# Kernel optimization log

Hardware: AMD Instinct MI355X
Metric: run time of the kernel (lower is better)

Reference implementation:

```python
import jax, jax.numpy as jnp
import numpy as np

W_BIT = 4
OUT_F = 11008
IN_F = 4096
K = 16


def unpack_sign(q_bytes):
    """q_bytes: [n_bytes] int32 holding uint8 values. Little-endian bit order.
    Returns float32 signs in {-1, +1} of shape [OUT_F, IN_F]."""
    bits = (q_bytes[:, None] >> jnp.arange(8, dtype=q_bytes.dtype)) & 1  # [n_bytes, 8]
    signs = (2 * bits - 1).astype(jnp.float32)
    return signs.reshape(OUT_F, IN_F)


def setup_inputs() -> dict:
    key = jax.random.key(0)
    k0, k1, k2, k3 = jax.random.split(key, 4)
    x = jax.random.normal(k0, (4, 2048, IN_F), dtype=jnp.float32)
    # packed sign bits: one byte stores 8 signs; OUT_F*IN_F//8 bytes per bit-plane
    qweight = jax.random.randint(k1, (W_BIT, OUT_F * IN_F // 8), 0, 256, dtype=jnp.int32)
    u = jax.random.normal(k2, (W_BIT, OUT_F, K), dtype=jnp.float32) * 0.05
    vt = jax.random.normal(k3, (W_BIT, K, IN_F), dtype=jnp.float32) * 0.05
    return {"x": x, "qweight": qweight, "u": u, "vt": vt}


def reference(x, qweight, u, vt):
    # Reconstruct full weight: w = sum_i sign_i * (u_i @ vt_i), then GEMM x @ w.T.
    # Loop over the small fixed w_bit count to avoid holding all [OUT,IN] bit-planes at once.
    w = jnp.zeros((OUT_F, IN_F), dtype=x.dtype)
    for i in range(W_BIT):
        signs = unpack_sign(qweight[i])            # [OUT_F, IN_F]
        w = w + signs * (u[i] @ vt[i])             # rank-K reconstruction masked by signs
    return x @ w.T                                  # [B, S, OUT_F]
```

## Files before the change

### kernel.cpp

```cpp
#include <hip/hip_runtime.h>
#include <hip/hip_bf16.h>

#define W_BIT 4
#define OUT_F 11008
#define IN_F 4096
#define KRANK 16
#define M_DIM 8192
#define QW_PLANE (OUT_F * IN_F / 8)

#define N_DIM OUT_F
#define K_DIM 4096
#define NT 64
#define NBN 43
#define RW_BLOCKS 5504
#define CV_BLOCKS 1024

typedef __attribute__((ext_vector_type(8))) short short8;
typedef __attribute__((ext_vector_type(4))) float f32x4;

__device__ __forceinline__ short f2bf(float f) {
    union { float f; unsigned u; } v;
    v.f = f;
    unsigned r = v.u + 0x7fffu + ((v.u >> 16) & 1u);
    return (short)(r >> 16);
}

__device__ __forceinline__ void async16(void* lds_p, const void* g) {
    __builtin_amdgcn_global_load_lds(
        (const __attribute__((address_space(1))) unsigned int*)g,
        (__attribute__((address_space(3))) unsigned int*)lds_p,
        16, 0, 0);
}

#define BAR() __builtin_amdgcn_s_barrier()
#define LGKM(n) do { asm volatile("s_waitcnt lgkmcnt(" #n ")" ::: "memory"); \
                     __builtin_amdgcn_sched_barrier(0); } while (0)
#define VMC(n) do { asm volatile("s_waitcnt vmcnt(" #n ")" ::: "memory"); \
                    __builtin_amdgcn_sched_barrier(0); } while (0)
#define PRIO1() __builtin_amdgcn_s_setprio(1)
#define PRIO0() __builtin_amdgcn_s_setprio(0)

#define DSR(DST, AV, IMM) \
    asm volatile("ds_read_b128 %0, %1 offset:%2" : "=v"(DST) : "v"(AV), "n"(IMM))

__global__ __launch_bounds__(256) void prep_kernel(
    const float* __restrict__ x, const int* __restrict__ qw,
    const float* __restrict__ u, const float* __restrict__ vt,
    short* __restrict__ xb, short* __restrict__ wb) {
    const int b = blockIdx.x;
    const int t = threadIdx.x;

    if (b >= RW_BLOCKS) {
        const int n8 = (M_DIM * IN_F) / 8;
        int tid = (b - RW_BLOCKS) * 256 + t;
        for (int i = tid; i < n8; i += CV_BLOCKS * 256) {
            f32x4 a = ((const f32x4*)x)[2 * i];
            f32x4 c = ((const f32x4*)x)[2 * i + 1];
            short8 o;
            o[0] = f2bf(a[0]); o[1] = f2bf(a[1]); o[2] = f2bf(a[2]); o[3] = f2bf(a[3]);
            o[4] = f2bf(c[0]); o[5] = f2bf(c[1]); o[6] = f2bf(c[2]); o[7] = f2bf(c[3]);
            ((short8*)xb)[i] = o;
        }
        return;
    }

    __shared__ float vts[64][128];
    __shared__ float us[64][64];

    const int c0 = (b & 31) * 128;
    const int o0 = (b >> 5) * 64;

    {
        const f32x4* vt4 = (const f32x4*)vt;
        const int l32 = t & 31;
        const int r0w = t >> 5;
#pragma unroll
        for (int j = 0; j < 8; ++j) {
            int row = r0w + j * 8;
            ((f32x4*)&vts[row][0])[l32] = vt4[(size_t)row * 1024 + (c0 >> 2) + l32];
        }
    }
    {
        const int o = t & 63, q = t >> 6;
#pragma unroll
        for (int i = 0; i < 4; ++i) {
            f32x4 v = ((const f32x4*)u)[((size_t)i * OUT_F + o0 + o) * 4 + q];
            us[i * 16 + q * 4 + 0][o] = v[0];
            us[i * 16 + q * 4 + 1][o] = v[1];
            us[i * 16 + q * 4 + 2][o] = v[2];
            us[i * 16 + q * 4 + 3][o] = v[3];
        }
    }
    __syncthreads();

    const int to = (t >> 4) * 4;
    const int tc = (t & 15) * 8;

    float wacc[4][8];
#pragma unroll
    for (int r = 0; r < 4; ++r)
#pragma unroll
        for (int c = 0; c < 8; ++c) wacc[r][c] = 0.f;

#pragma unroll
    for (int i = 0; i < W_BIT; ++i) {
        float dot[4][8];
#pragma unroll
        for (int r = 0; r < 4; ++r)
#pragma unroll
            for (int c = 0; c < 8; ++c) dot[r][c] = 0.f;
#pragma unroll
        for (int k = 0; k < KRANK; ++k) {
            f32x4 uv = *(const f32x4*)&us[i * 16 + k][to];
            f32x4 v0 = *(const f32x4*)&vts[i * 16 + k][tc];
            f32x4 v1 = *(const f32x4*)&vts[i * 16 + k][tc + 4];
#pragma unroll
            for (int r = 0; r < 4; ++r) {
#pragma unroll
                for (int c = 0; c < 4; ++c) {
                    dot[r][c]     += uv[r] * v0[c];
                    dot[r][c + 4] += uv[r] * v1[c];
                }
            }
        }
#pragma unroll
        for (int r = 0; r < 4; ++r) {
            unsigned byte = (unsigned)qw[i * QW_PLANE + (((o0 + to + r) * IN_F + c0 + tc) >> 3)];
#pragma unroll
            for (int c = 0; c < 8; ++c)
                wacc[r][c] += ((byte >> c) & 1u) ? dot[r][c] : -dot[r][c];
        }
    }
#pragma unroll
    for (int r = 0; r < 4; ++r) {
        short8 o8;
#pragma unroll
        for (int c = 0; c < 8; ++c) o8[c] = f2bf(wacc[r][c]);
        *(short8*)&wb[(size_t)(o0 + to + r) * IN_F + c0 + tc] = o8;
    }
}

__global__ __launch_bounds__(512, 2) void gemm256_kernel(
    const short* __restrict__ A, const short* __restrict__ B, float* __restrict__ C) {
    extern __shared__ short lds[];

    const int t = threadIdx.x;
    const int lane = t & 63, wid = t >> 6;
    const int wr = wid >> 2, wc = wid & 3;
    const int fr = lane & 15, fq = lane >> 4;

    const int bid = blockIdx.x;
    const int cpx = gridDim.x >> 3;
    const int swzb = (bid & 7) * cpx + (bid >> 3);
    const int bm = swzb / NBN, bn = swzb % NBN;
    const long row0 = (long)bm * 256, col0 = (long)bn * 256;

    const int colswz = (fq ^ ((fr >> 1) & 3)) * 8;
    const int aoff = (wr * 128 + fr) * 32 + colswz;
    const int boff = 32768 + (wc * 64 + fr) * 32 + colswz;

    const unsigned av = (unsigned)(size_t)((__attribute__((address_space(3))) short*)lds + aoff);
    const unsigned bv = (unsigned)(size_t)((__attribute__((address_space(3))) short*)lds + boff);

    const int srow = t >> 2;
    const int sswz = (((t & 3) ^ ((srow >> 1) & 3)) << 3);
    const short* pA0 = A + (row0 + srow) * (size_t)K_DIM + sswz;
    const short* pA1 = pA0 + (size_t)128 * K_DIM;
    const short* pB0 = B + (col0 + srow) * (size_t)K_DIM + sswz;
    const short* pB1 = pB0 + (size_t)128 * K_DIM;
    const int ldst0 = t * 8;

    f32x4 acc[8][4];
#pragma unroll
    for (int m = 0; m < 8; ++m)
#pragma unroll
        for (int n = 0; n < 4; ++n) acc[m][n] = (f32x4)0.f;

    short8 afA[4], afB[4], bf0[4], bf1[4];

#define STG(P0, P1, SLOT, OFFB) do {                                   \
    async16(&lds[(SLOT) + ldst0], (const char*)(P0) + (OFFB));         \
    async16(&lds[(SLOT) + 4096 + ldst0], (const char*)(P1) + (OFFB));  \
} while (0)

#define RDA(SET, KSLOT, MH) do {                                       \
    DSR(SET[0], av, ((KSLOT) + ((MH) * 4 + 0) * 512) * 2);             \
    DSR(SET[1], av, ((KSLOT) + ((MH) * 4 + 1) * 512) * 2);             \
    DSR(SET[2], av, ((KSLOT) + ((MH) * 4 + 2) * 512) * 2);             \
    DSR(SET[3], av, ((KSLOT) + ((MH) * 4 + 3) * 512) * 2);             \
} while (0)

#define RDB(DST, KSLOT) do {                                           \
    DSR(DST[0], bv, ((KSLOT) - 32768 + 0 * 512) * 2);                  \
    DSR(DST[1], bv, ((KSLOT) - 32768 + 1 * 512) * 2);                  \
    DSR(DST[2], bv, ((KSLOT) - 32768 + 2 * 512) * 2);                  \
    DSR(DST[3], bv, ((KSLOT) - 32768 + 3 * 512) * 2);                  \
} while (0)

#define MMA(AF, BF, MH) do { PRIO1();                                  \
    _Pragma("unroll") for (int m = 0; m < 4; ++m)                      \
        _Pragma("unroll") for (int n = 0; n < 4; ++n)                  \
            acc[(MH) * 4 + m][n] = __builtin_amdgcn_mfma_f32_16x16x32_bf16( \
                AF[m], BF[n], acc[(MH) * 4 + m][n], 0, 0, 0);          \
    PRIO0(); __builtin_amdgcn_sched_barrier(0); } while (0)

    STG(pA0, pA1, 0,     0);
    STG(pB0, pB1, 32768, 0);
    STG(pA0, pA1, 8192,  64);
    STG(pB0, pB1, 40960, 64);
    STG(pA0, pA1, 16384, 128);
    STG(pB0, pB1, 49152, 128);
    VMC(4);
    BAR();
    RDA(afA, 0, 0); RDB(bf0, 32768);

    for (int it = 0; it < 31; ++it) {
        RDA(afB, 0, 1);
        STG(pA0, pA1, 24576, 192);
        BAR(); LGKM(4); MMA(afA, bf0, 0);
        RDB(bf1, 40960); RDA(afA, 8192, 0);
        STG(pB0, pB1, 57344, 192);
        BAR(); LGKM(8); MMA(afB, bf0, 1);
        RDA(afB, 8192, 1);
        STG(pA0, pA1, 0, 256);
        BAR(); LGKM(4); MMA(afA, bf1, 0);
        STG(pB0, pB1, 32768, 256);
        VMC(4);
        RDB(bf0, 49152); RDA(afA, 16384, 0);
        BAR(); LGKM(8); MMA(afB, bf1, 1);

        RDA(afB, 16384, 1);
        STG(pA0, pA1, 8192, 320);
        BAR(); LGKM(4); MMA(afA, bf0, 0);
        RDB(bf1, 57344); RDA(afA, 24576, 0);
        STG(pB0, pB1, 40960, 320);
        BAR(); LGKM(8); MMA(afB, bf0, 1);
        RDA(afB, 24576, 1);
        STG(pA0, pA1, 16384, 384);
        BAR(); LGKM(4); MMA(afA, bf1, 0);
        STG(pB0, pB1, 49152, 384);
        VMC(4);
        RDB(bf0, 32768); RDA(afA, 0, 0);
        BAR(); LGKM(8); MMA(afB, bf1, 1);

        pA0 += 128; pA1 += 128; pB0 += 128; pB1 += 128;
    }

    RDA(afB, 0, 1);
    STG(pA0, pA1, 24576, 192);
    BAR(); LGKM(4); MMA(afA, bf0, 0);
    RDB(bf1, 40960); RDA(afA, 8192, 0);
    STG(pB0, pB1, 57344, 192);
    BAR(); LGKM(8); MMA(afB, bf0, 1);
    RDA(afB, 8192, 1);
    BAR(); LGKM(4); MMA(afA, bf1, 0);
    VMC(0);
    RDB(bf0, 49152); RDA(afA, 16384, 0);
    BAR(); LGKM(8); MMA(afB, bf1, 1);
    RDA(afB, 16384, 1);
    BAR(); LGKM(4); MMA(afA, bf0, 0);
    RDB(bf1, 57344); RDA(afA, 24576, 0);
    BAR(); LGKM(8); MMA(afB, bf0, 1);
    RDA(afB, 24576, 1);
    BAR(); LGKM(4); MMA(afA, bf1, 0);
    BAR(); LGKM(0); MMA(afB, bf1, 1);

#pragma unroll
    for (int m = 0; m < 8; ++m) {
#pragma unroll
        for (int n = 0; n < 4; ++n) {
            f32x4 v = acc[m][n];
            long r0 = row0 + wr * 128 + m * 16 + fq * 4;
            long cc = col0 + wc * 64 + n * 16 + fr;
#pragma unroll
            for (int jj = 0; jj < 4; ++jj)
                C[(size_t)(r0 + jj) * N_DIM + cc] = v[jj];
        }
    }
#undef STG
#undef RDA
#undef RDB
#undef MMA
}

extern "C" void kernel_launch(void* const* d_in, const int* in_sizes, int n_in,
                              void* d_out, int out_size, void* d_ws, size_t ws_size,
                              hipStream_t stream) {
    const float* x  = (const float*)d_in[0];
    const int*   qw = (const int*)d_in[1];
    const float* u  = (const float*)d_in[2];
    const float* vt = (const float*)d_in[3];
    float* out = (float*)d_out;

    const size_t wb_bytes = (size_t)OUT_F * IN_F * 2;
    short* wb = (short*)d_ws;
    short* xb = (short*)((char*)d_ws + wb_bytes);

    (void)hipFuncSetAttribute((const void*)gemm256_kernel,
                              hipFuncAttributeMaxDynamicSharedMemorySize, 131072);

    hipLaunchKernelGGL(prep_kernel, dim3(RW_BLOCKS + CV_BLOCKS), dim3(256), 0, stream,
                       x, qw, u, vt, xb, wb);
    hipLaunchKernelGGL(gemm256_kernel, dim3((M_DIM / 256) * (N_DIM / 256)), dim3(512), 131072,
                       stream, xb, wb, out);
}
```

Baseline: 855.9 us.

## Switch GEMM main loop to BK=64 double-buffered LDS tiles with 8-way swizzle

Reworks the bf16 GEMM mainloop from four 32-wide K slots to two 64-wide K stages (ping-pong), staging 64-column rows with an 8-group XOR swizzle and issuing two MFMAs per accumulator per quarter-tile. Intent is fewer barriers and prefetch phases per K step and larger loads per stage, cutting sync overhead. It adds more barriers per quadrant, waits for all LDS reads (lgkmcnt 0) before each MFMA block, and uses more fragment registers, which can reduce latency hiding.

```diff
diff --git a/kernel.cpp b/kernel.cpp
--- a/kernel.cpp
+++ b/kernel.cpp
@@ -10,7 +10,6 @@
 
 #define N_DIM OUT_F
 #define K_DIM 4096
-#define NT 64
 #define NBN 43
 #define RW_BLOCKS 5504
 #define CV_BLOCKS 1024
@@ -33,7 +32,7 @@
 }
 
 #define BAR() __builtin_amdgcn_s_barrier()
-#define LGKM(n) do { asm volatile("s_waitcnt lgkmcnt(" #n ")" ::: "memory"); \
+#define LGKM0() do { asm volatile("s_waitcnt lgkmcnt(0)" ::: "memory"); \
                      __builtin_amdgcn_sched_barrier(0); } while (0)
 #define VMC(n) do { asm volatile("s_waitcnt vmcnt(" #n ")" ::: "memory"); \
                     __builtin_amdgcn_sched_barrier(0); } while (0)
@@ -155,20 +154,19 @@
     const int bm = swzb / NBN, bn = swzb % NBN;
     const long row0 = (long)bm * 256, col0 = (long)bn * 256;
 
-    const int colswz = (fq ^ ((fr >> 1) & 3)) * 8;
-    const int aoff = (wr * 128 + fr) * 32 + colswz;
-    const int boff = 32768 + (wc * 64 + fr) * 32 + colswz;
-
-    const unsigned av = (unsigned)(size_t)((__attribute__((address_space(3))) short*)lds + aoff);
-    const unsigned bv = (unsigned)(size_t)((__attribute__((address_space(3))) short*)lds + boff);
-
-    const int srow = t >> 2;
-    const int sswz = (((t & 3) ^ ((srow >> 1) & 3)) << 3);
-    const short* pA0 = A + (row0 + srow) * (size_t)K_DIM + sswz;
-    const short* pA1 = pA0 + (size_t)128 * K_DIM;
-    const short* pB0 = B + (col0 + srow) * (size_t)K_DIM + sswz;
-    const short* pB1 = pB0 + (size_t)128 * K_DIM;
-    const int ldst0 = t * 8;
+    const int f7 = fr & 7;
+    const int g0 = fq ^ f7;
+    const int g1 = (4 + fq) ^ f7;
+    const int arow = (wr * 128 + fr) * 64;
+    const int brow = (wc * 64 + fr) * 64;
+    const unsigned av0 = (unsigned)(size_t)((__attribute__((address_space(3))) short*)lds + arow + g0 * 8);
+    const unsigned av1 = (unsigned)(size_t)((__attribute__((address_space(3))) short*)lds + arow + g1 * 8);
+    const unsigned bv0 = (unsigned)(size_t)((__attribute__((address_space(3))) short*)lds + 32768 + brow + g0 * 8);
+    const unsigned bv1 = (unsigned)(size_t)((__attribute__((address_space(3))) short*)lds + 32768 + brow + g1 * 8);
+
+    const int sswz = (((t & 7) ^ ((t >> 3) & 7)) << 3);
+    const short* pA = A + (row0 + (t >> 3)) * (size_t)K_DIM + sswz;
+    const short* pB = B + (col0 + (t >> 3)) * (size_t)K_DIM + sswz;
 
     f32x4 acc[8][4];
 #pragma unroll
@@ -176,94 +174,97 @@
 #pragma unroll
         for (int n = 0; n < 4; ++n) acc[m][n] = (f32x4)0.f;
 
-    short8 afA[4], afB[4], bf0[4], bf1[4];
-
-#define STG(P0, P1, SLOT, OFFB) do {                                   \
-    async16(&lds[(SLOT) + ldst0], (const char*)(P0) + (OFFB));         \
-    async16(&lds[(SLOT) + 4096 + ldst0], (const char*)(P1) + (OFFB));  \
-} while (0)
-
-#define RDA(SET, KSLOT, MH) do {                                       \
-    DSR(SET[0], av, ((KSLOT) + ((MH) * 4 + 0) * 512) * 2);             \
-    DSR(SET[1], av, ((KSLOT) + ((MH) * 4 + 1) * 512) * 2);             \
-    DSR(SET[2], av, ((KSLOT) + ((MH) * 4 + 2) * 512) * 2);             \
-    DSR(SET[3], av, ((KSLOT) + ((MH) * 4 + 3) * 512) * 2);             \
-} while (0)
-
-#define RDB(DST, KSLOT) do {                                           \
-    DSR(DST[0], bv, ((KSLOT) - 32768 + 0 * 512) * 2);                  \
-    DSR(DST[1], bv, ((KSLOT) - 32768 + 1 * 512) * 2);                  \
-    DSR(DST[2], bv, ((KSLOT) - 32768 + 2 * 512) * 2);                  \
-    DSR(DST[3], bv, ((KSLOT) - 32768 + 3 * 512) * 2);                  \
-} while (0)
-
-#define MMA(AF, BF, MH) do { PRIO1();                                  \
-    _Pragma("unroll") for (int m = 0; m < 4; ++m)                      \
-        _Pragma("unroll") for (int n = 0; n < 4; ++n)                  \
-            acc[(MH) * 4 + m][n] = __builtin_amdgcn_mfma_f32_16x16x32_bf16( \
-                AF[m], BF[n], acc[(MH) * 4 + m][n], 0, 0, 0);          \
+    short8 a0[8], a1[8], b0[4], b1[4];
+
+#define STGA(P, H, OFFB) do {                                               \
+    async16(&lds[(P) * 16384 + (2 * (H)) * 4096 + t * 8],                   \
+            (const char*)(pA + (size_t)(2 * (H)) * 64 * K_DIM) + (OFFB));   \
+    async16(&lds[(P) * 16384 + (2 * (H) + 1) * 4096 + t * 8],               \
+            (const char*)(pA + (size_t)(2 * (H) + 1) * 64 * K_DIM) + (OFFB)); \
+} while (0)
+#define STGB(P, H, OFFB) do {                                               \
+    async16(&lds[32768 + (P) * 16384 + (2 * (H)) * 4096 + t * 8],           \
+            (const char*)(pB + (size_t)(2 * (H)) * 64 * K_DIM) + (OFFB));   \
+    async16(&lds[32768 + (P) * 16384 + (2 * (H) + 1) * 4096 + t * 8],       \
+            (const char*)(pB + (size_t)(2 * (H) + 1) * 64 * K_DIM) + (OFFB)); \
+} while (0)
+
+#define RDA(SET, P, MH) do {                                                \
+    DSR(SET[0], av0, ((P) * 16384 + (MH) * 4096 + 0 * 1024) * 2);           \
+    DSR(SET[1], av0, ((P) * 16384 + (MH) * 4096 + 1 * 1024) * 2);           \
+    DSR(SET[2], av0, ((P) * 16384 + (MH) * 4096 + 2 * 1024) * 2);           \
+    DSR(SET[3], av0, ((P) * 16384 + (MH) * 4096 + 3 * 1024) * 2);           \
+    DSR(SET[4], av1, ((P) * 16384 + (MH) * 4096 + 0 * 1024) * 2);           \
+    DSR(SET[5], av1, ((P) * 16384 + (MH) * 4096 + 1 * 1024) * 2);           \
+    DSR(SET[6], av1, ((P) * 16384 + (MH) * 4096 + 2 * 1024) * 2);           \
+    DSR(SET[7], av1, ((P) * 16384 + (MH) * 4096 + 3 * 1024) * 2);           \
+} while (0)
+
+#define RDB(SET, P, NH) do {                                                \
+    DSR(SET[0], bv0, ((P) * 16384 + (NH) * 2048 + 0 * 1024) * 2);           \
+    DSR(SET[1], bv0, ((P) * 16384 + (NH) * 2048 + 1 * 1024) * 2);           \
+    DSR(SET[2], bv1, ((P) * 16384 + (NH) * 2048 + 0 * 1024) * 2);           \
+    DSR(SET[3], bv1, ((P) * 16384 + (NH) * 2048 + 1 * 1024) * 2);           \
+} while (0)
+
+#define MMAQ(ASET, BSET, MH, NH) do { PRIO1();                              \
+    _Pragma("unroll") for (int m = 0; m < 4; ++m)                           \
+        _Pragma("unroll") for (int n = 0; n < 2; ++n) {                     \
+            acc[(MH) * 4 + m][(NH) * 2 + n] =                               \
+                __builtin_amdgcn_mfma_f32_16x16x32_bf16(                    \
+                    ASET[m], BSET[n], acc[(MH) * 4 + m][(NH) * 2 + n], 0, 0, 0); \
+            acc[(MH) * 4 + m][(NH) * 2 + n] =                               \
+                __builtin_amdgcn_mfma_f32_16x16x32_bf16(                    \
+                    ASET[4 + m], BSET[2 + n], acc[(MH) * 4 + m][(NH) * 2 + n], 0, 0, 0); \
+        }                                                                   \
     PRIO0(); __builtin_amdgcn_sched_barrier(0); } while (0)
 
-    STG(pA0, pA1, 0,     0);
-    STG(pB0, pB1, 32768, 0);
-    STG(pA0, pA1, 8192,  64);
-    STG(pB0, pB1, 40960, 64);
-    STG(pA0, pA1, 16384, 128);
-    STG(pB0, pB1, 49152, 128);
+#define TILE(P, OFFB, OFFA) do {                                            \
+                                                          \
+    RDA(a0, P, 0); RDB(b0, P, 0);                                           \
+    STGB(1 - (P), 0, OFFB);                                                 \
+    BAR(); LGKM0(); MMAQ(a0, b0, 0, 0); BAR();                              \
+                                                          \
+    RDA(a1, P, 1);                                                          \
+    STGB(1 - (P), 1, OFFB);                                                 \
+    BAR(); LGKM0(); MMAQ(a1, b0, 1, 0); BAR();                              \
+                                                          \
+    RDB(b1, P, 1);                                                          \
+    STGA(P, 0, OFFA);                                                       \
+    BAR(); LGKM0(); MMAQ(a1, b1, 1, 1); BAR();                              \
+                             \
+    STGA(P, 1, OFFA);                                                       \
+    BAR(); MMAQ(a0, b1, 0, 1); VMC(4); BAR();                               \
+} while (0)
+
+    STGA(0, 0, 0); STGA(0, 1, 0);
+    STGB(0, 0, 0); STGB(0, 1, 0);
+    STGA(1, 0, 128); STGA(1, 1, 128);
     VMC(4);
     BAR();
-    RDA(afA, 0, 0); RDB(bf0, 32768);
 
     for (int it = 0; it < 31; ++it) {
-        RDA(afB, 0, 1);
-        STG(pA0, pA1, 24576, 192);
-        BAR(); LGKM(4); MMA(afA, bf0, 0);
-        RDB(bf1, 40960); RDA(afA, 8192, 0);
-        STG(pB0, pB1, 57344, 192);
-        BAR(); LGKM(8); MMA(afB, bf0, 1);
-        RDA(afB, 8192, 1);
-        STG(pA0, pA1, 0, 256);
-        BAR(); LGKM(4); MMA(afA, bf1, 0);
-        STG(pB0, pB1, 32768, 256);
-        VMC(4);
-        RDB(bf0, 49152); RDA(afA, 16384, 0);
-        BAR(); LGKM(8); MMA(afB, bf1, 1);
-
-        RDA(afB, 16384, 1);
-        STG(pA0, pA1, 8192, 320);
-        BAR(); LGKM(4); MMA(afA, bf0, 0);
-        RDB(bf1, 57344); RDA(afA, 24576, 0);
-        STG(pB0, pB1, 40960, 320);
-        BAR(); LGKM(8); MMA(afB, bf0, 1);
-        RDA(afB, 24576, 1);
-        STG(pA0, pA1, 16384, 384);
-        BAR(); LGKM(4); MMA(afA, bf1, 0);
-        STG(pB0, pB1, 49152, 384);
-        VMC(4);
-        RDB(bf0, 32768); RDA(afA, 0, 0);
-        BAR(); LGKM(8); MMA(afB, bf1, 1);
-
-        pA0 += 128; pA1 += 128; pB0 += 128; pB1 += 128;
-    }
-
-    RDA(afB, 0, 1);
-    STG(pA0, pA1, 24576, 192);
-    BAR(); LGKM(4); MMA(afA, bf0, 0);
-    RDB(bf1, 40960); RDA(afA, 8192, 0);
-    STG(pB0, pB1, 57344, 192);
-    BAR(); LGKM(8); MMA(afB, bf0, 1);
-    RDA(afB, 8192, 1);
-    BAR(); LGKM(4); MMA(afA, bf1, 0);
-    VMC(0);
-    RDB(bf0, 49152); RDA(afA, 16384, 0);
-    BAR(); LGKM(8); MMA(afB, bf1, 1);
-    RDA(afB, 16384, 1);
-    BAR(); LGKM(4); MMA(afA, bf0, 0);
-    RDB(bf1, 57344); RDA(afA, 24576, 0);
-    BAR(); LGKM(8); MMA(afB, bf0, 1);
-    RDA(afB, 24576, 1);
-    BAR(); LGKM(4); MMA(afA, bf1, 0);
-    BAR(); LGKM(0); MMA(afB, bf1, 1);
+        TILE(0, 128, 256);
+        TILE(1, 256, 384);
+        pA += 128; pB += 128;
+    }
+
+    RDA(a0, 0, 0); RDB(b0, 0, 0);
+    STGB(1, 0, 128);
+    BAR(); LGKM0(); MMAQ(a0, b0, 0, 0); BAR();
+    RDA(a1, 0, 1);
+    STGB(1, 1, 128);
+    BAR(); LGKM0(); MMAQ(a1, b0, 1, 0); BAR();
+    RDB(b1, 0, 1);
+    BAR(); LGKM0(); MMAQ(a1, b1, 1, 1); BAR();
+    BAR(); MMAQ(a0, b1, 0, 1); VMC(0); BAR();
+    RDA(a0, 1, 0); RDB(b0, 1, 0);
+    BAR(); LGKM0(); MMAQ(a0, b0, 0, 0); BAR();
+    RDA(a1, 1, 1);
+    BAR(); LGKM0(); MMAQ(a1, b0, 1, 0); BAR();
+    RDB(b1, 1, 1);
+    BAR(); LGKM0(); MMAQ(a1, b1, 1, 1); BAR();
+    BAR(); MMAQ(a0, b1, 0, 1);
 
 #pragma unroll
     for (int m = 0; m < 8; ++m) {
@@ -277,10 +278,12 @@
                 C[(size_t)(r0 + jj) * N_DIM + cc] = v[jj];
         }
     }
-#undef STG
+#undef STGA
+#undef STGB
 #undef RDA
 #undef RDB
-#undef MMA
+#undef MMAQ
+#undef TILE
 }
 
 extern "C" void kernel_launch(void* const* d_in, const int* in_sizes, int n_in,
```

After: 822.2 us. 3.9% less time.
